# Kernel optimization log

Hardware: AMD Instinct MI355X
Metric: run time of the kernel (lower is better)

Reference implementation:

```python
import jax, jax.numpy as jnp
import numpy as np

H = 4    # heads
DK = 5   # d_k = d_model // h = 20 // 4
D = 20   # d_model


def _proj(x, W, b):
    # x: [B,S,D] -> [B,H,S,DK]
    B, S, _ = x.shape
    y = x @ W.T + b
    return y.reshape(B, S, H, DK).transpose(0, 2, 1, 3)


def _attn(q, k, v, mask4):
    # q,k,v: [B,H,S,DK]; mask4: [B,1,1,S]
    scores = jnp.einsum('bhqd,bhkd->bhqk', q, k) / jnp.sqrt(jnp.asarray(DK, q.dtype))
    scores = jnp.where(mask4 == 0, jnp.asarray(-1e9, q.dtype), scores)
    p = jax.nn.softmax(scores, axis=-1)  # dropout omitted (eval mode)
    return jnp.einsum('bhqk,bhkd->bhqd', p, v)


def setup_inputs() -> dict:
    key = jax.random.key(0)
    ks = jax.random.split(key, 12)
    B, S = 8, 2048
    scale = 1.0 / np.sqrt(D)
    inp = {
        'query': jax.random.normal(ks[0], (B, S, D), dtype=jnp.float32),
        'key': jax.random.normal(ks[1], (B, S, D), dtype=jnp.float32),
        'value': jax.random.normal(ks[2], (B, S, D), dtype=jnp.float32),
        'mask': jax.random.randint(ks[3], (B, S), 0, 2, dtype=jnp.int32),
    }
    for i in range(4):
        inp[f'W{i}'] = jax.random.normal(ks[4 + 2 * i], (D, D), dtype=jnp.float32) * scale
        inp[f'b{i}'] = jax.random.normal(ks[5 + 2 * i], (D,), dtype=jnp.float32) * 0.01
    return inp


def reference(query, key, value, mask, W0, b0, W1, b1, W2, b2, W3, b3):
    B, S, _ = query.shape
    mask4 = mask[:, None, None, :]  # [B,1,1,S]
    # Six permuted (arg-to-linear0, arg-to-linear1, arg-to-linear2) variants,
    # exactly as the torch forward: (q,k,k),(k,q,q),(q,v,v),(v,q,q),(k,v,v),(v,k,k)
    triples = [
        (query, key, key), (key, query, query),
        (query, value, value), (value, query, query),
        (key, value, value), (value, key, key),
    ]
    out = None
    for a, bb, c in triples:
        o = _attn(_proj(a, W0, b0), _proj(bb, W1, b1), _proj(c, W2, b2), mask4)
        out = o if out is None else out + o
    # merge heads: [B,H,S,DK] -> [B,S,D]
    out = out.transpose(0, 2, 1, 3).reshape(B, S, H * DK)
    return out @ W3.T + b3
```

## Files before the change

### kernel.cpp

```cpp
#include <hip/hip_runtime.h>
#include <cstdint>
#include <cstddef>

#define B    8
#define SEQ  2048
#define H    4
#define DKN  5
#define DIM  20
#define PRE8 8
#define SENTB ((short)0xC2FC)
#define ONEB  ((short)0x3F80)
#define B128  ((short)0x4300)
#define PBIASM 12599162.0f

typedef short short8 __attribute__((ext_vector_type(8)));
typedef float f32x16 __attribute__((ext_vector_type(16)));

static __device__ __forceinline__ unsigned short bf16b(float x) {
    union { float f; unsigned u; } v; v.f = x;
    unsigned r = v.u + 0x7FFFu + ((v.u >> 16) & 1u);
    return (unsigned short)(r >> 16);
}
static __device__ __forceinline__ float bf16f(unsigned short h) {
    union { unsigned u; float f; } v; v.u = ((unsigned)h) << 16;
    return v.f;
}
static __device__ __forceinline__ unsigned pk_pbits(float ta, float tb) {
    unsigned ia, ib;
    __builtin_memcpy(&ia, &ta, 4);
    __builtin_memcpy(&ib, &tb, 4);
    return __builtin_amdgcn_perm(ib, ia, 0x05040100u);
}
static __device__ __forceinline__ int sig32(int t) {
    return (t & 19) | ((t & 4) << 1) | ((t & 8) >> 1);
}

typedef unsigned __attribute__((address_space(1))) gas_u32;
typedef unsigned __attribute__((address_space(3))) las_u32;
static __device__ __forceinline__ void glds16(const void* g, void* l) {
    __builtin_amdgcn_global_load_lds((const gas_u32*)g, (las_u32*)l, 16, 0, 0);
}


__global__ __launch_bounds__(256) void proj_kernel(
    const float* __restrict__ q, const float* __restrict__ k, const float* __restrict__ v,
    const float* __restrict__ W0, const float* __restrict__ b0,
    const float* __restrict__ W1, const float* __restrict__ b1,
    const float* __restrict__ W2, const float* __restrict__ b2,
    const int* __restrict__ mask,
    short* __restrict__ Qt, short* __restrict__ Kt, short* __restrict__ Vt,
    int* __restrict__ meta)
{
    __shared__ float Ws[3][DIM * DIM];
    __shared__ float bsh[3][DIM];
    __shared__ int   widx[256];
    __shared__ int   cntS;

    int tid = threadIdx.x;
    int blk = blockIdx.x;
    int w   = blk & 7;  blk >>= 3;
    int h   = blk & 3;  blk >>= 2;
    int bb  = blk & 7;  blk >>= 3;
    int x   = blk;
    int s0  = w * 256;

    for (int i = tid; i < DIM * DIM; i += 256) {
        Ws[0][i] = W0[i]; Ws[1][i] = W1[i]; Ws[2][i] = W2[i];
    }
    if (tid < DIM) { bsh[0][tid] = b0[tid]; bsh[1][tid] = b1[tid]; bsh[2][tid] = b2[tid]; }

    if (tid < 64) {
        const int* mrow = mask + bb * SEQ;
        int base = 0;
        for (int ch = 0; ch < SEQ; ch += 64) {
            int mv = mrow[ch + tid];
            unsigned long long bal = __ballot(mv != 0);
            int pos = base + (int)__popcll(bal & ((1ull << tid) - 1ull));
            if (mv && pos >= s0 && pos < s0 + 256) widx[pos - s0] = ch + tid;
            base += (int)__popcll(bal);
        }
        if (tid == 0) {
            cntS = base;
            if (x == 0 && h == 0 && w == 0) meta[bb] = base;
        }
    }
    __syncthreads();

    int  cnt   = cntS;
    int  c     = s0 + tid;
    bool valid = c < cnt;
    int  gs    = valid ? widx[tid] : 0;

    const float QSC = 0.44721359549995793f * 1.4426950408889634f * 128.0f;
    const float* base = (x == 0) ? q : ((x == 1) ? k : v);

    float xq[DIM], xg[DIM];
    {
        const float4* r4 = (const float4*)(base + (size_t)(bb * SEQ + c) * DIM);
        const float4* g4 = (const float4*)(base + (size_t)(bb * SEQ + gs) * DIM);
        #pragma unroll
        for (int i = 0; i < 5; ++i) {
            float4 a = r4[i], g = g4[i];
            xq[i*4+0]=a.x; xq[i*4+1]=a.y; xq[i*4+2]=a.z; xq[i*4+3]=a.w;
            xg[i*4+0]=g.x; xg[i*4+1]=g.y; xg[i*4+2]=g.z; xg[i*4+3]=g.w;
        }
    }

    #define DOT20(xv, t, j, dst) {                                        \
        float acc_ = bsh[t][j];                                           \
        const float4* wr_ = (const float4*)&Ws[t][(j) * DIM];             \
        _Pragma("unroll")                                                 \
        for (int i4 = 0; i4 < 5; ++i4) {                                  \
            float4 w_ = wr_[i4];                                          \
            acc_ += (xv)[i4*4+0]*w_.x + (xv)[i4*4+1]*w_.y                 \
                  + (xv)[i4*4+2]*w_.z + (xv)[i4*4+3]*w_.w;                \
        }                                                                 \
        dst = acc_;                                                       \
    }

    size_t row = ((size_t)(x * B + bb) * H + h) * SEQ + c;

    short8 qhi = {0, 0, 0, 0, 0, B128, 0, 0};
    short8 qlo = {0, 0, 0, 0, 0, 0, 0, 0};
    #pragma unroll
    for (int d = 0; d < DKN; ++d) {
        float y; DOT20(xq, 0, h * DKN + d, y);
        y *= QSC;
        unsigned short hb = bf16b(y);
        qhi[d] = (short)hb;
        qlo[d] = (short)bf16b(y - bf16f(hb));
    }
    ((short8*)Qt)[row * 2 + 0] = qhi;
    ((short8*)Qt)[row * 2 + 1] = qlo;

    short8 rk = {0, 0, 0, 0, 0, valid ? (short)0 : SENTB, 0, 0};
    if (valid) {
        #pragma unroll
        for (int d = 0; d < DKN; ++d) {
            float y; DOT20(xg, 1, h * DKN + d, y);
            rk[d] = (short)bf16b(y);
        }
    }
    ((short8*)Kt)[row] = rk;

    if (valid) {
        size_t vb = ((size_t)(x * B + bb) * H + h) * 8 * SEQ;
        size_t vcell = vb + (size_t)(c >> 5) * 256 + sig32(c & 31);
        #pragma unroll
        for (int d = 0; d < DKN; ++d) {
            float y; DOT20(xg, 2, h * DKN + d, y);
            Vt[vcell + (size_t)d * 32] = (short)bf16b(y);
        }
        Vt[vcell + (size_t)5 * 32] = ONEB;
    }
}

__global__ __launch_bounds__(128, 4) void attn_kernel(
    const short* __restrict__ Qt, const short* __restrict__ Kt,
    const short* __restrict__ Vt, const int* __restrict__ meta,
    float* __restrict__ pre)
{
    __shared__ char lds[2][2][2048];

    int wv   = threadIdx.x >> 6;
    int lane = threadIdx.x & 63;
    int l31  = lane & 31, half = lane >> 5;

    int wid  = blockIdx.x;
    int qtq  = wid / 192;
    int grp  = wid - qtq * 192;
    int h    = grp & 3;  grp >>= 2;
    int b    = grp & 7;  grp >>= 3;
    int p    = grp;
    int a    = (0x212010 >> (4 * p)) & 0xF;
    int kv   = (0x120201 >> (4 * p)) & 0xF;
    int qt0  = qtq * 4 + wv * 2;

    int cnt  = meta[b];
    int kend = (cnt + 63) & ~63;

    const short* Qb  = Qt + ((size_t)(a  * B + b) * H + h) * SEQ * 16;
    const char*  Kst = (const char*)(Kt + ((size_t)(kv * B + b) * H + h) * SEQ * 8);
    const char*  Vst = (const char*)(Vt + ((size_t)(kv * B + b) * H + h) * 8 * SEQ);

    char* myl = &lds[wv][0][0];
    int koff = l31 * 16;
    int voff = 1024 + (l31 & 7) * 64 + half * 16;

    short8 qf[2];
    f32x16 acc[2];
    f32x16 zc = {0.f,0.f,0.f,0.f,0.f,0.f,0.f,0.f,0.f,0.f,0.f,0.f,0.f,0.f,0.f,0.f};
    f32x16 sb = {PBIASM,PBIASM,PBIASM,PBIASM,PBIASM,PBIASM,PBIASM,PBIASM,
                 PBIASM,PBIASM,PBIASM,PBIASM,PBIASM,PBIASM,PBIASM,PBIASM};
    #pragma unroll
    for (int t = 0; t < 2; ++t) {
        int qb = (qt0 + t) * 32;
        qf[t]  = *(const short8*)(Qb + (size_t)(qb + l31) * 16 + half * 8);
        acc[t] = zc;
    }

    glds16(Kst + lane * 16, myl);
    glds16(Vst + lane * 16, myl + 1024);

    #define PVSTEP(D, VA, VC, ACC) {                                          \
        unsigned p0_[4], p1_[4];                                              \
        _Pragma("unroll")                                                     \
        for (int r = 0; r < 4; ++r) {                                         \
            p0_[r] = pk_pbits(D[2 * r],     D[2 * r + 1]);                    \
            p1_[r] = pk_pbits(D[2 * r + 8], D[2 * r + 9]);                    \
        }                                                                     \
        short8 f0_, f1_;                                                      \
        __builtin_memcpy(&f0_, p0_, 16);                                      \
        __builtin_memcpy(&f1_, p1_, 16);                                      \
        ACC = __builtin_amdgcn_mfma_f32_32x32x16_bf16(VA, f0_, ACC, 0, 0, 0); \
        ACC = __builtin_amdgcn_mfma_f32_32x32x16_bf16(VC, f1_, ACC, 0, 0, 0); \
    }

    int buf = 0;
    for (int c0 = 0; c0 < kend; c0 += 64) {
        size_t c1b = (size_t)(c0 + 64) * 16;
        char* nb = myl + ((buf ^ 1) << 11);
        glds16(Kst + c1b + lane * 16, nb);
        glds16(Vst + c1b + lane * 16, nb + 1024);

        __builtin_amdgcn_sched_barrier(0);
        asm volatile("s_waitcnt vmcnt(2)" ::: "memory");
        __builtin_amdgcn_sched_barrier(0);

        const char* cb = myl + (buf << 11);
        short8 kfA = *(const short8*)(cb + koff);
        short8 vaA = *(const short8*)(cb + voff);
        short8 vcA = *(const short8*)(cb + voff + 32);

        __builtin_amdgcn_s_setprio(1);
        #pragma unroll
        for (int t = 0; t < 2; ++t) {
            f32x16 dA = __builtin_amdgcn_mfma_f32_32x32x16_bf16(kfA, qf[t], sb, 0, 0, 0);
            PVSTEP(dA, vaA, vcA, acc[t]);
        }
        __builtin_amdgcn_s_setprio(0);

        short8 kfB = *(const short8*)(cb + koff + 512);
        short8 vaB = *(const short8*)(cb + voff + 512);
        short8 vcB = *(const short8*)(cb + voff + 544);

        __builtin_amdgcn_s_setprio(1);
        #pragma unroll
        for (int t = 0; t < 2; ++t) {
            f32x16 dB = __builtin_amdgcn_mfma_f32_32x32x16_bf16(kfB, qf[t], sb, 0, 0, 0);
            PVSTEP(dB, vaB, vcB, acc[t]);
        }
        __builtin_amdgcn_s_setprio(0);

        buf ^= 1;
    }

    float* base0 = pre + (((size_t)p * B + b) * H + h) * SEQ * PRE8;
    #pragma unroll
    for (int t = 0; t < 2; ++t) {
        int qb = (qt0 + t) * 32;
        float lv  = __shfl(acc[t][1], 32 + l31, 64);
        float inv = 1.0f / lv;
        float* dst = base0 + (size_t)(qb + l31) * PRE8;
        if (half == 0)
            *(float4*)dst = make_float4(acc[t][0]*inv, acc[t][1]*inv,
                                        acc[t][2]*inv, acc[t][3]*inv);
        else
            dst[4] = acc[t][0] * inv;
    }
}

__global__ __launch_bounds__(64) void final_kernel(
    const float* __restrict__ pre,
    const float* __restrict__ W3, const float* __restrict__ b3,
    float* __restrict__ out)
{
    __shared__ float Ws[DIM * DIM];
    __shared__ float bs[DIM];
    int tid = threadIdx.x;
    for (int i = tid; i < DIM * DIM; i += 64) Ws[i] = W3[i];
    if (tid < DIM) bs[tid] = b3[tid];
    __syncthreads();

    int g = blockIdx.x * 64 + tid;
    int b = g / SEQ;
    int s = g - b * SEQ;

    float x[DIM];
    #pragma unroll
    for (int i = 0; i < DIM; ++i) x[i] = 0.f;

    for (int p = 0; p < 6; ++p) {
        #pragma unroll
        for (int h = 0; h < H; ++h) {
            const float* sr = pre + (((size_t)p * B + b) * H + h) * SEQ * PRE8
                                  + (size_t)s * PRE8;
            float4 a = *(const float4*)sr;
            float  a4 = sr[4];
            x[h * DKN + 0] += a.x; x[h * DKN + 1] += a.y; x[h * DKN + 2] += a.z;
            x[h * DKN + 3] += a.w; x[h * DKN + 4] += a4;
        }
    }

    float y[DIM];
    for (int j = 0; j < DIM; ++j) {
        float acc = bs[j];
        const float4* wr = (const float4*)&Ws[j * DIM];
        #pragma unroll
        for (int i4 = 0; i4 < 5; ++i4) {
            float4 w = wr[i4];
            acc += x[i4*4+0]*w.x + x[i4*4+1]*w.y + x[i4*4+2]*w.z + x[i4*4+3]*w.w;
        }
        y[j] = acc;
    }
    float4* dst = (float4*)(out + (size_t)(b * SEQ + s) * DIM);
    #pragma unroll
    for (int j4 = 0; j4 < 5; ++j4)
        dst[j4] = make_float4(y[j4*4+0], y[j4*4+1], y[j4*4+2], y[j4*4+3]);
}

extern "C" void kernel_launch(void* const* d_in, const int* in_sizes, int n_in,
                              void* d_out, int out_size, void* d_ws, size_t ws_size,
                              hipStream_t stream) {
    const float* q    = (const float*)d_in[0];
    const float* k    = (const float*)d_in[1];
    const float* v    = (const float*)d_in[2];
    const int*   mask = (const int*)d_in[3];
    const float* W0 = (const float*)d_in[4];  const float* b0 = (const float*)d_in[5];
    const float* W1 = (const float*)d_in[6];  const float* b1 = (const float*)d_in[7];
    const float* W2 = (const float*)d_in[8];  const float* b2 = (const float*)d_in[9];
    const float* W3 = (const float*)d_in[10]; const float* b3 = (const float*)d_in[11];

    const size_t NROW = (size_t)3 * B * H * SEQ;
    short* Qt = (short*)d_ws;
    short* Kt = Qt + NROW * 16;
    short* Vt = Kt + NROW * 8;
    float* pre = (float*)(Vt + NROW * 8);
    int*   meta = (int*)(pre + (size_t)6 * B * H * SEQ * PRE8);
    float* out = (float*)d_out;

    proj_kernel<<<dim3(3 * B * H * (SEQ / 256)), dim3(256), 0, stream>>>(
        q, k, v, W0, b0, W1, b1, W2, b2, mask, Qt, Kt, Vt, meta);
    attn_kernel<<<dim3(6 * B * H * 16), dim3(128), 0, stream>>>(
        Qt, Kt, Vt, meta, pre);
    final_kernel<<<dim3(B * SEQ / 64), dim3(64), 0, stream>>>(pre, W3, b3, out);
}
```

Before: 137.2 us.

## Share each K/V stream across the two permutations that use it

The attention kernel now groups the six (query-source, kv-source) permutations by kv source, so each block processes two query sources against the same K/V tiles. K/V are loaded into LDS once and reused by both query sets, which halves the K/V traffic and the grid size. In exchange each wave holds twice the accumulators and Q fragments, so launch bounds drop from 4 to 3 blocks per SM and occupancy falls. Fewer blocks may also hurt load balance.

```diff
diff --git a/kernel.cpp b/kernel.cpp
--- a/kernel.cpp
+++ b/kernel.cpp
@@ -155,7 +155,7 @@
     }
 }
 
-__global__ __launch_bounds__(128, 4) void attn_kernel(
+__global__ __launch_bounds__(128, 3) void attn_kernel(
     const short* __restrict__ Qt, const short* __restrict__ Kt,
     const short* __restrict__ Vt, const int* __restrict__ meta,
     float* __restrict__ pre)
@@ -167,36 +167,41 @@
     int l31  = lane & 31, half = lane >> 5;
 
     int wid  = blockIdx.x;
-    int qtq  = wid / 192;
-    int grp  = wid - qtq * 192;
+    int qtq  = wid / 96;
+    int grp  = wid - qtq * 96;
     int h    = grp & 3;  grp >>= 2;
     int b    = grp & 7;  grp >>= 3;
-    int p    = grp;
-    int a    = (0x212010 >> (4 * p)) & 0xF;
-    int kv   = (0x120201 >> (4 * p)) & 0xF;
+    int kvi  = grp;
+    int aA = (0x001 >> (4 * kvi)) & 0xF;
+    int aB = (0x122 >> (4 * kvi)) & 0xF;
+    int pA = (0x201 >> (4 * kvi)) & 0xF;
+    int pB = (0x453 >> (4 * kvi)) & 0xF;
     int qt0  = qtq * 4 + wv * 2;
 
     int cnt  = meta[b];
     int kend = (cnt + 63) & ~63;
 
-    const short* Qb  = Qt + ((size_t)(a  * B + b) * H + h) * SEQ * 16;
-    const char*  Kst = (const char*)(Kt + ((size_t)(kv * B + b) * H + h) * SEQ * 8);
-    const char*  Vst = (const char*)(Vt + ((size_t)(kv * B + b) * H + h) * 8 * SEQ);
+    const short* QbA = Qt + ((size_t)(aA * B + b) * H + h) * SEQ * 16;
+    const short* QbB = Qt + ((size_t)(aB * B + b) * H + h) * SEQ * 16;
+    const char*  Kst = (const char*)(Kt + ((size_t)(kvi * B + b) * H + h) * SEQ * 8);
+    const char*  Vst = (const char*)(Vt + ((size_t)(kvi * B + b) * H + h) * 8 * SEQ);
 
     char* myl = &lds[wv][0][0];
     int koff = l31 * 16;
     int voff = 1024 + (l31 & 7) * 64 + half * 16;
 
-    short8 qf[2];
-    f32x16 acc[2];
+    short8 qf[2][2];
+    f32x16 acc[2][2];
     f32x16 zc = {0.f,0.f,0.f,0.f,0.f,0.f,0.f,0.f,0.f,0.f,0.f,0.f,0.f,0.f,0.f,0.f};
     f32x16 sb = {PBIASM,PBIASM,PBIASM,PBIASM,PBIASM,PBIASM,PBIASM,PBIASM,
                  PBIASM,PBIASM,PBIASM,PBIASM,PBIASM,PBIASM,PBIASM,PBIASM};
     #pragma unroll
     for (int t = 0; t < 2; ++t) {
-        int qb = (qt0 + t) * 32;
-        qf[t]  = *(const short8*)(Qb + (size_t)(qb + l31) * 16 + half * 8);
-        acc[t] = zc;
+        size_t qrow = (size_t)((qt0 + t) * 32 + l31) * 16 + half * 8;
+        qf[0][t] = *(const short8*)(QbA + qrow);
+        qf[1][t] = *(const short8*)(QbB + qrow);
+        acc[0][t] = zc;
+        acc[1][t] = zc;
     }
 
     glds16(Kst + lane * 16, myl);
@@ -234,9 +239,13 @@
 
         __builtin_amdgcn_s_setprio(1);
         #pragma unroll
-        for (int t = 0; t < 2; ++t) {
-            f32x16 dA = __builtin_amdgcn_mfma_f32_32x32x16_bf16(kfA, qf[t], sb, 0, 0, 0);
-            PVSTEP(dA, vaA, vcA, acc[t]);
+        for (int pr = 0; pr < 2; ++pr) {
+            #pragma unroll
+            for (int t = 0; t < 2; ++t) {
+                f32x16 dA = __builtin_amdgcn_mfma_f32_32x32x16_bf16(
+                    kfA, qf[pr][t], sb, 0, 0, 0);
+                PVSTEP(dA, vaA, vcA, acc[pr][t]);
+            }
         }
         __builtin_amdgcn_s_setprio(0);
 
@@ -246,27 +255,35 @@
 
         __builtin_amdgcn_s_setprio(1);
         #pragma unroll
+        for (int pr = 0; pr < 2; ++pr) {
+            #pragma unroll
+            for (int t = 0; t < 2; ++t) {
+                f32x16 dB = __builtin_amdgcn_mfma_f32_32x32x16_bf16(
+                    kfB, qf[pr][t], sb, 0, 0, 0);
+                PVSTEP(dB, vaB, vcB, acc[pr][t]);
+            }
+        }
+        __builtin_amdgcn_s_setprio(0);
+
+        buf ^= 1;
+    }
+
+    #pragma unroll
+    for (int pr = 0; pr < 2; ++pr) {
+        int p = pr ? pB : pA;
+        float* base0 = pre + (((size_t)p * B + b) * H + h) * SEQ * PRE8;
+        #pragma unroll
         for (int t = 0; t < 2; ++t) {
-            f32x16 dB = __builtin_amdgcn_mfma_f32_32x32x16_bf16(kfB, qf[t], sb, 0, 0, 0);
-            PVSTEP(dB, vaB, vcB, acc[t]);
-        }
-        __builtin_amdgcn_s_setprio(0);
-
-        buf ^= 1;
-    }
-
-    float* base0 = pre + (((size_t)p * B + b) * H + h) * SEQ * PRE8;
-    #pragma unroll
-    for (int t = 0; t < 2; ++t) {
-        int qb = (qt0 + t) * 32;
-        float lv  = __shfl(acc[t][1], 32 + l31, 64);
-        float inv = 1.0f / lv;
-        float* dst = base0 + (size_t)(qb + l31) * PRE8;
-        if (half == 0)
-            *(float4*)dst = make_float4(acc[t][0]*inv, acc[t][1]*inv,
-                                        acc[t][2]*inv, acc[t][3]*inv);
-        else
-            dst[4] = acc[t][0] * inv;
+            int qb = (qt0 + t) * 32;
+            float lv  = __shfl(acc[pr][t][1], 32 + l31, 64);
+            float inv = 1.0f / lv;
+            float* dst = base0 + (size_t)(qb + l31) * PRE8;
+            if (half == 0)
+                *(float4*)dst = make_float4(acc[pr][t][0]*inv, acc[pr][t][1]*inv,
+                                            acc[pr][t][2]*inv, acc[pr][t][3]*inv);
+            else
+                dst[4] = acc[pr][t][0] * inv;
+        }
     }
 }
 
@@ -341,7 +358,7 @@
 
     proj_kernel<<<dim3(3 * B * H * (SEQ / 256)), dim3(256), 0, stream>>>(
         q, k, v, W0, b0, W1, b1, W2, b2, mask, Qt, Kt, Vt, meta);
-    attn_kernel<<<dim3(6 * B * H * 16), dim3(128), 0, stream>>>(
+    attn_kernel<<<dim3(3 * B * H * 16), dim3(128), 0, stream>>>(
         Qt, Kt, Vt, meta, pre);
     final_kernel<<<dim3(B * SEQ / 64), dim3(64), 0, stream>>>(pre, W3, b3, out);
 }
```

Result: slower. 141.0 us (+2.8%).
